# Performance work log

Measured on AMD Instinct MI355X. Metric: run time of the kernel, lower is better.

The kernel has to match this reference:

```python
import jax, jax.numpy as jnp
import numpy as np

BETA_MIN, BETA_MAX = 0.01, 0.995
EPS_DELTA, EPS_RMS = 1e-6, 1e-5


def _rmsnorm(x, w):
    ms = jnp.mean(x * x, axis=-1, keepdims=True)
    return x * jax.lax.rsqrt(ms + EPS_RMS) * w


def _delta_scan(q, k, v, beta, mask, bb1, bb2):
    # q, k, v: [B, S, D]; beta, mask: [B, S, 1]; bb1, bb2: scalars
    phi_q = jax.nn.elu(q) + 1.0
    phi_k = jax.nn.elu(k) + 1.0
    b1_base = jnp.clip(jax.nn.sigmoid(bb1), BETA_MIN, BETA_MAX)
    b2_base = jnp.clip(jax.nn.sigmoid(bb2), BETA_MIN, BETA_MAX)
    B, S, D = q.shape

    def step(carry, inp):
        H1, H2, Z1, Z2 = carry
        qt, kt, vt, bt, mt = inp  # qt/kt/vt: [B,D], bt/mt: [B,1]
        bin_t = jnp.clip(bt, BETA_MIN, BETA_MAX)
        b1 = jnp.clip(b1_base * bin_t, BETA_MIN, BETA_MAX)  # [B,1]
        b2 = jnp.clip(b2_base * bin_t, BETA_MIN, BETA_MAX)
        kv = jnp.einsum('bd,be->bde', kt, vt) * mt[:, :, None]  # [B,D,D]
        H1 = H1 * b1[:, :, None] + kv
        H2 = H2 * b2[:, :, None] + kv
        km = kt * mt
        Z1 = Z1 * b1 + km
        Z2 = Z2 * b2 + km
        num = jnp.einsum('bd,bde->be', qt, H1 + H2)
        den = jnp.maximum(jnp.sum(qt * (Z1 + Z2), axis=-1, keepdims=True), EPS_DELTA)
        return (H1, H2, Z1, Z2), num / den * mt

    init = (jnp.zeros((B, D, D), q.dtype), jnp.zeros((B, D, D), q.dtype),
            jnp.zeros((B, D), q.dtype), jnp.zeros((B, D), q.dtype))
    xs = tuple(a.swapaxes(0, 1) for a in (phi_q, phi_k, v, beta, mask))
    _, outs = jax.lax.scan(step, init, xs)
    return outs.swapaxes(0, 1)  # [B, S, D]


def setup_inputs() -> dict:
    key = jax.random.key(0)
    B, S, Dm, H = 4, 2048, 512, 8
    ks = jax.random.split(key, 8)
    scale = float(1.0 / np.sqrt(Dm))
    return {
        'x': jax.random.normal(ks[0], (B, S, Dm), jnp.float32),
        'mask': jnp.ones((B, S), jnp.float32),
        'Wq': jax.random.normal(ks[1], (Dm, Dm), jnp.float32) * scale,
        'Wk': jax.random.normal(ks[2], (Dm, Dm), jnp.float32) * scale,
        'Wv': jax.random.normal(ks[3], (Dm, Dm), jnp.float32) * scale,
        'Wb': jax.random.normal(ks[4], (H, Dm), jnp.float32) * scale,
        'bb': jnp.full((H,), 1.5, jnp.float32),
        'Wo': jax.random.normal(ks[5], (Dm, Dm), jnp.float32) * scale,
        'bo': jnp.zeros((Dm,), jnp.float32),
        'ln_w': jnp.ones((Dm,), jnp.float32),
        'recency': jnp.zeros((H,), jnp.float32),
        'base_beta_1': jnp.asarray(2.0, jnp.float32),
        'base_beta_2': jnp.asarray(3.0, jnp.float32),
    }


def reference(x, mask, Wq, Wk, Wv, Wb, bb, Wo, bo, ln_w, recency,
              base_beta_1, base_beta_2):
    B, S, Dm = x.shape
    H = recency.shape[0]
    d = Dm // H
    h = _rmsnorm(x, ln_w)
    q = h @ Wq.T
    k = h @ Wk.T
    v = h @ Wv.T
    # input-conditioned gate with per-head recency bias  -> [B, S, H]
    beta = jax.nn.sigmoid(h @ Wb.T + bb + recency)

    def to_heads(t):  # [B,S,Dm] -> [B*H, S, d]
        return t.reshape(B, S, H, d).transpose(0, 2, 1, 3).reshape(B * H, S, d)

    qh, kh, vh = to_heads(q), to_heads(k), to_heads(v)
    betah = beta.transpose(0, 2, 1).reshape(B * H, S, 1)
    maskh = jnp.broadcast_to(mask[:, None, :, None], (B, H, S, 1)).reshape(B * H, S, 1)
    o = _delta_scan(qh, kh, vh, betah, maskh, base_beta_1, base_beta_2)
    o = o.reshape(B, H, S, d).transpose(0, 2, 1, 3).reshape(B, S, Dm)
    return x + (o @ Wo.T + bo)
```

## Files before the change

kernel.cpp:

```cpp
#include <hip/hip_runtime.h>
#include <stdint.h>

typedef unsigned short u16;
typedef short bf16x8 __attribute__((ext_vector_type(8)));
typedef unsigned short u16x8 __attribute__((ext_vector_type(8)));
typedef unsigned short u16x4 __attribute__((ext_vector_type(4)));
typedef float f32x4 __attribute__((ext_vector_type(4)));

#define S_ 2048
#define DM 512
#define DH 64
#define CL 64
#define NCH 32

#define SW(r, sc) ((r) * 72 + ((sc) ^ (((r) & 7) << 3)))

__device__ __forceinline__ float b2f(u16 u) { return __uint_as_float(((unsigned)u) << 16); }
__device__ __forceinline__ u16 f2b(float f) {
    unsigned v = __float_as_uint(f);
    unsigned r = v + 0x7fffu + ((v >> 16) & 1u);
    return (u16)(r >> 16);
}
__device__ __forceinline__ float phi_elu(float x) { return x > 0.f ? x + 1.f : __expf(x); }
__device__ __forceinline__ float clip01(float v) { return fminf(fmaxf(v, 0.01f), 0.995f); }

__device__ __forceinline__ void gload16(const u16* g, u16* l) {
    __builtin_amdgcn_global_load_lds((const __attribute__((address_space(1))) void*)g,
                                     (__attribute__((address_space(3))) void*)l, 16, 0, 0);
}

__global__ __launch_bounds__(256) void k_rbw(const float* __restrict__ x, const float* __restrict__ lnw,
                                             const float* __restrict__ Wb, const float* __restrict__ bb,
                                             const float* __restrict__ rec, const float* __restrict__ bb1p,
                                             const float* __restrict__ bb2p, u16* __restrict__ h,
                                             float* __restrict__ lb1, float* __restrict__ lb2,
                                             const float* __restrict__ Wq, const float* __restrict__ Wk,
                                             const float* __restrict__ Wv, const float* __restrict__ Wo,
                                             u16* __restrict__ wcat, u16* __restrict__ wo) {
    if (blockIdx.x >= 2048) {
        int idx = (blockIdx.x - 2048) * 256 + threadIdx.x;
        int e0 = idx << 2;
        if (e0 < 1536 * 512) {
            int r = e0 >> 9, ccol = e0 & 511;
            const float* src = (r < 512) ? (Wq + (size_t)r * 512)
                             : (r < 1024) ? (Wk + (size_t)(r - 512) * 512)
                                          : (Wv + (size_t)(r - 1024) * 512);
            float4 v = *(const float4*)(src + ccol);
            u16x4 o = {f2b(v.x), f2b(v.y), f2b(v.z), f2b(v.w)};
            *(u16x4*)(wcat + e0) = o;
        } else {
            int e = e0 - 1536 * 512;
            float4 v = *(const float4*)(Wo + e);
            u16x4 o = {f2b(v.x), f2b(v.y), f2b(v.z), f2b(v.w)};
            *(u16x4*)(wo + e) = o;
        }
        return;
    }
    int wave = threadIdx.x >> 6, lane = threadIdx.x & 63;
    int row = blockIdx.x * 4 + wave;
    const float* xr = x + (size_t)row * DM + lane * 8;
    float4 v0 = *(const float4*)xr;
    float4 v1 = *(const float4*)(xr + 4);
    float ss = v0.x * v0.x + v0.y * v0.y + v0.z * v0.z + v0.w * v0.w +
               v1.x * v1.x + v1.y * v1.y + v1.z * v1.z + v1.w * v1.w;
    #pragma unroll
    for (int off = 32; off; off >>= 1) ss += __shfl_xor(ss, off, 64);
    float sc = rsqrtf(ss * (1.f / DM) + 1e-5f);
    const float* wr_ = lnw + lane * 8;
    float4 w0 = *(const float4*)wr_;
    float4 w1 = *(const float4*)(wr_ + 4);
    float hv[8];
    hv[0] = v0.x * sc * w0.x; hv[1] = v0.y * sc * w0.y;
    hv[2] = v0.z * sc * w0.z; hv[3] = v0.w * sc * w0.w;
    hv[4] = v1.x * sc * w1.x; hv[5] = v1.y * sc * w1.y;
    hv[6] = v1.z * sc * w1.z; hv[7] = v1.w * sc * w1.w;
    u16x8 o;
    #pragma unroll
    for (int j = 0; j < 8; j++) o[j] = f2b(hv[j]);
    *(u16x8*)(h + (size_t)row * DM + lane * 8) = o;
    float acc[8];
    #pragma unroll
    for (int hd = 0; hd < 8; hd++) {
        const float* wp = Wb + hd * DM + lane * 8;
        float4 a0 = *(const float4*)wp;
        float4 a1 = *(const float4*)(wp + 4);
        acc[hd] = hv[0] * a0.x + hv[1] * a0.y + hv[2] * a0.z + hv[3] * a0.w +
                  hv[4] * a1.x + hv[5] * a1.y + hv[6] * a1.z + hv[7] * a1.w;
    }
    #pragma unroll
    for (int hd = 0; hd < 8; hd++) {
        #pragma unroll
        for (int off = 32; off; off >>= 1) acc[hd] += __shfl_xor(acc[hd], off, 64);
    }
    if (lane == 0) {
        float b1b = clip01(1.f / (1.f + __expf(-bb1p[0])));
        float b2b = clip01(1.f / (1.f + __expf(-bb2p[0])));
        int b = row >> 11, s = row & 2047;
        #pragma unroll
        for (int hd = 0; hd < 8; hd++) {
            float logit = acc[hd] + bb[hd] + rec[hd];
            float beta = 1.f / (1.f + __expf(-logit));
            float bin = clip01(beta);
            float b1 = clip01(b1b * bin);
            float b2 = clip01(b2b * bin);
            size_t o2 = (size_t)((b << 3) + hd) * S_ + s;
            lb1[o2] = log2f(b1);
            lb2[o2] = log2f(b2);
        }
    }
}

template<int MODE, int NT, int BM>
__global__ __launch_bounds__(BM * 2) void k_gemm(const u16* __restrict__ A, const u16* __restrict__ Bw, int K,
                                                 const float* __restrict__ mask, u16* __restrict__ qh,
                                                 u16* __restrict__ kh, u16* __restrict__ vh,
                                                 const float* __restrict__ xres, const float* __restrict__ bo,
                                                 float* __restrict__ outp) {
    constexpr int THREADS = BM * 2;
    constexpr int RPC = THREADS / 8;
    constexpr int ACALLS = BM / RPC;
    constexpr int BCALLS = 128 / RPC;
    __shared__ u16 SH[BM * 64 + 128 * 64];
    u16* As = SH;
    u16* Bs = SH + BM * 64;
    int tid = threadIdx.x;
    int lane = tid & 63, w = tid >> 6;
    int wr = w >> 1, wc = w & 1;
    int hwid = blockIdx.y * gridDim.x + blockIdx.x;
    int nwg = gridDim.x * NT;
    int q8 = nwg >> 3;
    int logical = (hwid & 7) * q8 + (hwid >> 3);
    int mTile = logical / NT, nTile = logical % NT;
    int m0 = mTile * BM, n0 = nTile * 128;
    f32x4 acc[4][4] = {};
    int r0 = tid >> 3;
    int swc8 = ((lane & 7) ^ (lane >> 3)) << 3;
    const u16* gA0 = A + (size_t)(m0 + r0) * K + swc8;
    const u16* gB0 = Bw + (size_t)(n0 + r0) * K + swc8;
    u16* lA = As + w * 512;
    u16* lB = Bs + w * 512;
    int l15 = lane & 15;
    int kgrp = lane >> 4;
    for (int k0 = 0; k0 < K; k0 += 64) {
        if (k0) __syncthreads();
        #pragma unroll
        for (int rb = 0; rb < ACALLS; rb++)
            gload16(gA0 + (size_t)rb * RPC * K + k0, lA + rb * RPC * 64);
        #pragma unroll
        for (int rb = 0; rb < BCALLS; rb++)
            gload16(gB0 + (size_t)rb * RPC * K + k0, lB + rb * RPC * 64);
        __syncthreads();
        #pragma unroll
        for (int kk = 0; kk < 2; kk++) {
            int kg = kgrp + kk * 4;
            int cg = (kg ^ (l15 & 7)) << 3;
            bf16x8 af[4], bfr[4];
            #pragma unroll
            for (int m = 0; m < 4; m++) af[m] = *(const bf16x8*)&As[(wr * 64 + m * 16 + l15) * 64 + cg];
            #pragma unroll
            for (int n = 0; n < 4; n++) bfr[n] = *(const bf16x8*)&Bs[(wc * 64 + n * 16 + l15) * 64 + cg];
            #pragma unroll
            for (int m = 0; m < 4; m++)
                #pragma unroll
                for (int n = 0; n < 4; n++)
                    acc[m][n] = __builtin_amdgcn_mfma_f32_16x16x32_bf16(af[m], bfr[n], acc[m][n], 0, 0, 0);
        }
    }
    __syncthreads();
    if constexpr (MODE == 0) {
        int mat = n0 >> 9;
        int cb = n0 & 511;
        u16* basep = (mat == 0) ? qh : (mat == 1) ? kh : vh;
        #pragma unroll
        for (int P = 0; P < BM / 64; P++) {
            if (wr == P) {
                #pragma unroll
                for (int m = 0; m < 4; m++)
                    #pragma unroll
                    for (int n = 0; n < 4; n++)
                        #pragma unroll
                        for (int r = 0; r < 4; r++) {
                            int rl = m * 16 + ((lane >> 4) << 2) + r;
                            int colL = wc * 64 + n * 16 + l15;
                            SH[rl * 140 + colL] = f2b(acc[m][n][r]);
                        }
            }
            __syncthreads();
            {
                int rl = tid >> 2;
                int gr = m0 + P * 64 + rl;
                int b = gr >> 11, s = gr & 2047;
                float mv = (mat == 1) ? mask[(b << 11) + s] : 1.f;
                #pragma unroll
                for (int cc = 0; cc < 4; cc++) {
                    int cl = ((tid & 3) << 5) + (cc << 3);
                    u16x8 vv = *(const u16x8*)&SH[rl * 140 + cl];
                    int f = cb + cl;
                    int hh = f >> 6, j = f & 63;
                    u16* dst = basep + ((size_t)(b * 8 + hh) * S_ + s) * DH + j;
                    if (mat == 2) {
                        *(u16x8*)dst = vv;
                    } else {
                        u16x8 ov;
                        #pragma unroll
                        for (int e = 0; e < 8; e++) {
                            float v = b2f(vv[e]);
                            ov[e] = f2b(phi_elu(v) * mv);
                        }
                        *(u16x8*)dst = ov;
                    }
                }
            }
            __syncthreads();
        }
    } else {
        float* SF = (float*)SH;
        constexpr int PQN = BM / 32;
        #pragma unroll
        for (int Pq = 0; Pq < PQN; Pq++) {
            if (wr == (Pq >> 1)) {
                int mbase = (Pq & 1) * 2;
                #pragma unroll
                for (int mm = 0; mm < 2; mm++)
                    #pragma unroll
                    for (int n = 0; n < 4; n++)
                        #pragma unroll
                        for (int r = 0; r < 4; r++) {
                            int rl = mm * 16 + ((lane >> 4) << 2) + r;
                            int colL = wc * 64 + n * 16 + l15;
                            SF[rl * 136 + colL] = acc[mbase + mm][n][r];
                        }
            }
            __syncthreads();
            {
                int rl, col0;
                if constexpr (THREADS == 256) { rl = tid >> 3; col0 = (tid & 7) << 4; }
                else                          { rl = tid >> 2; col0 = (tid & 3) << 5; }
                constexpr int NCC = (THREADS == 256) ? 4 : 8;
                int gr = m0 + Pq * 32 + rl;
                const float* xr = xres + (size_t)gr * DM + n0 + col0;
                float* orow = outp + (size_t)gr * DM + n0 + col0;
                #pragma unroll
                for (int cc = 0; cc < NCC; cc++) {
                    int cl = col0 + (cc << 2);
                    float4 v = *(const float4*)&SF[rl * 136 + cl];
                    float4 xv = *(const float4*)(xr + (cc << 2));
                    float4 bv = *(const float4*)(bo + n0 + cl);
                    float4 ov = {v.x + xv.x + bv.x, v.y + xv.y + bv.y,
                                 v.z + xv.z + bv.z, v.w + xv.w + bv.w};
                    *(float4*)(orow + (cc << 2)) = ov;
                }
            }
            __syncthreads();
        }
    }
}

__global__ __launch_bounds__(256) void k_pass1(const u16* __restrict__ kh, const u16* __restrict__ vh,
                                               const float* __restrict__ lb1, const float* __restrict__ lb2,
                                               u16* __restrict__ S1b, u16* __restrict__ S2b,
                                               float* __restrict__ z1, float* __restrict__ z2,
                                               float* __restrict__ P1, float* __restrict__ P2) {
    __shared__ u16 Kw1[64 * 72];
    __shared__ u16 Kw2[64 * 72];
    __shared__ u16 Vt[64 * 72];
    __shared__ float Ls1[64], Ls2[64];
    int tid = threadIdx.x;
    int bh = blockIdx.x >> 5, c = blockIdx.x & 31;
    int wave = tid >> 6, lane = tid & 63;
    size_t base = ((size_t)bh * S_ + c * CL) * DH;
    if (wave == 0) {
        float v = lb1[(size_t)bh * S_ + c * CL + lane];
        #pragma unroll
        for (int d = 1; d < 64; d <<= 1) { float o = __shfl_up(v, d, 64); if (lane >= d) v += o; }
        Ls1[lane] = v;
    } else if (wave == 1) {
        float v = lb2[(size_t)bh * S_ + c * CL + lane];
        #pragma unroll
        for (int d = 1; d < 64; d <<= 1) { float o = __shfl_up(v, d, 64); if (lane >= d) v += o; }
        Ls2[lane] = v;
    }
    int ss = tid & 63, i0 = (tid >> 6) << 4;
    const u16* kr = kh + base + (size_t)ss * DH + i0;
    u16x8 kk0 = *(const u16x8*)kr;
    u16x8 kk1 = *(const u16x8*)(kr + 8);
    {
        const u16* vr = vh + base + (size_t)ss * DH + i0;
        u16x8 vv0 = *(const u16x8*)vr;
        u16x8 vv1 = *(const u16x8*)(vr + 8);
        #pragma unroll
        for (int j = 0; j < 8; j++) {
            Vt[SW(i0 + j, ss)] = vv0[j];
            Vt[SW(i0 + 8 + j, ss)] = vv1[j];
        }
    }
    __syncthreads();
    float w1 = exp2f(Ls1[63] - Ls1[ss]);
    float w2 = exp2f(Ls2[63] - Ls2[ss]);
    #pragma unroll
    for (int j = 0; j < 8; j++) {
        float k0 = b2f(kk0[j]), k1 = b2f(kk1[j]);
        Kw1[SW(i0 + j, ss)] = f2b(w1 * k0);
        Kw2[SW(i0 + j, ss)] = f2b(w2 * k0);
        Kw1[SW(i0 + 8 + j, ss)] = f2b(w1 * k1);
        Kw2[SW(i0 + 8 + j, ss)] = f2b(w2 * k1);
    }
    if (tid == 0) { P1[blockIdx.x] = exp2f(Ls1[63]); P2[blockIdx.x] = exp2f(Ls2[63]); }
    __syncthreads();
    int l15 = lane & 15, kh8 = (lane >> 4) << 3;
    int j0 = wave << 4;
    bf16x8 vf0 = *(const bf16x8*)&Vt[SW(j0 + l15, kh8)];
    bf16x8 vf1 = *(const bf16x8*)&Vt[SW(j0 + l15, 32 + kh8)];
    f32x4 a1[4], a2[4];
    #pragma unroll
    for (int it = 0; it < 4; it++) { a1[it] = (f32x4){0,0,0,0}; a2[it] = (f32x4){0,0,0,0}; }
    #pragma unroll
    for (int it = 0; it < 4; it++) {
        int ir = (it << 4) + l15;
        bf16x8 b0 = *(const bf16x8*)&Kw1[SW(ir, kh8)];
        bf16x8 b1 = *(const bf16x8*)&Kw1[SW(ir, 32 + kh8)];
        a1[it] = __builtin_amdgcn_mfma_f32_16x16x32_bf16(vf0, b0, a1[it], 0, 0, 0);
        a1[it] = __builtin_amdgcn_mfma_f32_16x16x32_bf16(vf1, b1, a1[it], 0, 0, 0);
        bf16x8 c0 = *(const bf16x8*)&Kw2[SW(ir, kh8)];
        bf16x8 c1 = *(const bf16x8*)&Kw2[SW(ir, 32 + kh8)];
        a2[it] = __builtin_amdgcn_mfma_f32_16x16x32_bf16(vf0, c0, a2[it], 0, 0, 0);
        a2[it] = __builtin_amdgcn_mfma_f32_16x16x32_bf16(vf1, c1, a2[it], 0, 0, 0);
    }
    {
        int iz = tid >> 2, sg = tid & 3;
        u16x8 x0 = *(const u16x8*)&Kw1[SW(iz, sg << 4)];
        u16x8 x1 = *(const u16x8*)&Kw1[SW(iz, (sg << 4) + 8)];
        u16x8 y0 = *(const u16x8*)&Kw2[SW(iz, sg << 4)];
        u16x8 y1 = *(const u16x8*)&Kw2[SW(iz, (sg << 4) + 8)];
        float z1v = 0.f, z2v = 0.f;
        #pragma unroll
        for (int j = 0; j < 8; j++) {
            z1v += b2f(x0[j]) + b2f(x1[j]);
            z2v += b2f(y0[j]) + b2f(y1[j]);
        }
        z1v += __shfl_xor(z1v, 1, 64); z1v += __shfl_xor(z1v, 2, 64);
        z2v += __shfl_xor(z2v, 1, 64); z2v += __shfl_xor(z2v, 2, 64);
        if (sg == 0) {
            z1[(size_t)blockIdx.x * 64 + iz] = z1v;
            z2[(size_t)blockIdx.x * 64 + iz] = z2v;
        }
    }
    int jr0 = j0 + ((lane >> 4) << 2);
    size_t so = (size_t)blockIdx.x * 4096;
    #pragma unroll
    for (int it = 0; it < 4; it++) {
        int ii = (it << 4) + l15;
        #pragma unroll
        for (int r = 0; r < 4; r++) {
            S1b[so + (size_t)(jr0 + r) * 64 + ii] = f2b(a1[it][r]);
            S2b[so + (size_t)(jr0 + r) * 64 + ii] = f2b(a2[it][r]);
        }
    }
}

__global__ __launch_bounds__(256) void k_pass2(u16* __restrict__ S1b, u16* __restrict__ S2b,
                                               float* __restrict__ z1, float* __restrict__ z2,
                                               const float* __restrict__ P1, const float* __restrict__ P2) {
    int blk = blockIdx.x;
    if (blk < 512) {
        int bh = blk >> 4;
        int e = ((blk & 15) << 8) + threadIdx.x;
        float c1 = 0.f, c2 = 0.f;
        #pragma unroll 4
        for (int c = 0; c < NCH; c++) {
            int bc = bh * NCH + c;
            size_t idx = (size_t)bc * 4096 + e;
            float p1 = P1[bc], p2 = P2[bc];
            float t1 = b2f(S1b[idx]); S1b[idx] = f2b(c1); c1 = c1 * p1 + t1;
            float t2 = b2f(S2b[idx]); S2b[idx] = f2b(c2); c2 = c2 * p2 + t2;
        }
    } else {
        int bh = ((blk - 512) << 2) + (threadIdx.x >> 6);
        int e = threadIdx.x & 63;
        float y1 = 0.f, y2 = 0.f;
        #pragma unroll 4
        for (int c = 0; c < NCH; c++) {
            int bc = bh * NCH + c;
            size_t zi = (size_t)bc * 64 + e;
            float p1 = P1[bc], p2 = P2[bc];
            float t1 = z1[zi]; z1[zi] = y1; y1 = y1 * p1 + t1;
            float t2 = z2[zi]; z2[zi] = y2; y2 = y2 * p2 + t2;
        }
    }
}

__global__ __launch_bounds__(256) void k_pass3(const u16* __restrict__ qh, const u16* __restrict__ kh,
                                               const u16* __restrict__ vh, const float* __restrict__ lb1,
                                               const float* __restrict__ lb2, const u16* __restrict__ S1b,
                                               const u16* __restrict__ S2b, const float* __restrict__ z1,
                                               const float* __restrict__ z2, const float* __restrict__ mask,
                                               u16* __restrict__ obf) {
    __shared__ u16 Vt[64 * 72];
    __shared__ u16 AWs[64 * 72];
    __shared__ float Ls1[64], Ls2[64], dens[64], qZ1[64], qZ2[64];
    int tid = threadIdx.x;
    int bh = blockIdx.x >> 5, c = blockIdx.x & 31;
    int wave = tid >> 6, lane = tid & 63;
    size_t base = ((size_t)bh * S_ + c * CL) * DH;
    if (wave == 0) {
        float v = lb1[(size_t)bh * S_ + c * CL + lane];
        #pragma unroll
        for (int d = 1; d < 64; d <<= 1) { float o = __shfl_up(v, d, 64); if (lane >= d) v += o; }
        Ls1[lane] = v;
    } else if (wave == 1) {
        float v = lb2[(size_t)bh * S_ + c * CL + lane];
        #pragma unroll
        for (int d = 1; d < 64; d <<= 1) { float o = __shfl_up(v, d, 64); if (lane >= d) v += o; }
        Ls2[lane] = v;
    }
    {
        int ss = tid & 63, i0 = (tid >> 6) << 4;
        const u16* vr = vh + base + (size_t)ss * DH + i0;
        u16x8 vv0 = *(const u16x8*)vr;
        u16x8 vv1 = *(const u16x8*)(vr + 8);
        #pragma unroll
        for (int j = 0; j < 8; j++) {
            Vt[SW(i0 + j, ss)] = vv0[j];
            Vt[SW(i0 + 8 + j, ss)] = vv1[j];
        }
    }
    {
        int t = tid >> 2, g = tid & 3;
        const u16* qp = qh + base + (size_t)t * DH + (g << 4);
        u16x8 q0 = *(const u16x8*)qp;
        u16x8 q1 = *(const u16x8*)(qp + 8);
        const float* z1p = z1 + (size_t)blockIdx.x * 64 + (g << 4);
        const float* z2p = z2 + (size_t)blockIdx.x * 64 + (g << 4);
        float az1 = 0.f, az2 = 0.f;
        #pragma unroll
        for (int m = 0; m < 8; m++) {
            float qv0 = b2f(q0[m]), qv1 = b2f(q1[m]);
            az1 += qv0 * z1p[m] + qv1 * z1p[m + 8];
            az2 += qv0 * z2p[m] + qv1 * z2p[m + 8];
        }
        az1 += __shfl_xor(az1, 1, 64); az1 += __shfl_xor(az1, 2, 64);
        az2 += __shfl_xor(az2, 1, 64); az2 += __shfl_xor(az2, 2, 64);
        if (g == 0) { qZ1[t] = az1; qZ2[t] = az2; }
    }
    int l15 = lane & 15, kh8 = (lane >> 4) << 3;
    int t0 = wave << 4;
    const u16* qb = qh + base + (size_t)(t0 + l15) * DH;
    bf16x8 qf0 = *(const bf16x8*)(qb + kh8);
    bf16x8 qf1 = *(const bf16x8*)(qb + 32 + kh8);
    f32x4 accA[4];
    #pragma unroll
    for (int st = 0; st < 4; st++) accA[st] = (f32x4){0, 0, 0, 0};
    #pragma unroll
    for (int st = 0; st < 4; st++) {
        const u16* kb = kh + base + (size_t)((st << 4) + l15) * DH;
        bf16x8 kf0 = *(const bf16x8*)(kb + kh8);
        bf16x8 kf1 = *(const bf16x8*)(kb + 32 + kh8);
        accA[st] = __builtin_amdgcn_mfma_f32_16x16x32_bf16(qf0, kf0, accA[st], 0, 0, 0);
        accA[st] = __builtin_amdgcn_mfma_f32_16x16x32_bf16(qf1, kf1, accA[st], 0, 0, 0);
    }
    __syncthreads();
    int trow = t0 + ((lane >> 4) << 2);
    float l1t[4], l2t[4];
    #pragma unroll
    for (int r = 0; r < 4; r++) { l1t[r] = Ls1[trow + r]; l2t[r] = Ls2[trow + r]; }
    float rs[4] = {0.f, 0.f, 0.f, 0.f};
    #pragma unroll
    for (int st = 0; st < 4; st++) {
        int s = (st << 4) + l15;
        float s1 = Ls1[s], s2 = Ls2[s];
        #pragma unroll
        for (int r = 0; r < 4; r++) {
            float w = 0.f;
            if (s <= trow + r) w = exp2f(l1t[r] - s1) + exp2f(l2t[r] - s2);
            u16 awb = f2b(accA[st][r] * w);
            AWs[SW(trow + r, s)] = awb;
            rs[r] += b2f(awb);
        }
    }
    #pragma unroll
    for (int off = 1; off < 16; off <<= 1) {
        #pragma unroll
        for (int r = 0; r < 4; r++) rs[r] += __shfl_xor(rs[r], off, 64);
    }
    if (l15 == 0) {
        #pragma unroll
        for (int r = 0; r < 4; r++) dens[trow + r] = rs[r];
    }
    __syncthreads();
    bf16x8 awf0 = *(const bf16x8*)&AWs[SW(t0 + l15, kh8)];
    bf16x8 awf1 = *(const bf16x8*)&AWs[SW(t0 + l15, 32 + kh8)];
    const u16* h1g = S1b + (size_t)blockIdx.x * 4096;
    const u16* h2g = S2b + (size_t)blockIdx.x * 4096;
    f32x4 accO[4], accC1[4], accC2[4];
    #pragma unroll
    for (int jt = 0; jt < 4; jt++) {
        accO[jt] = (f32x4){0, 0, 0, 0};
        accC1[jt] = (f32x4){0, 0, 0, 0};
        accC2[jt] = (f32x4){0, 0, 0, 0};
    }
    #pragma unroll
    for (int jt = 0; jt < 4; jt++) {
        int jr = (jt << 4) + l15;
        bf16x8 v0 = *(const bf16x8*)&Vt[SW(jr, kh8)];
        bf16x8 v1 = *(const bf16x8*)&Vt[SW(jr, 32 + kh8)];
        accO[jt] = __builtin_amdgcn_mfma_f32_16x16x32_bf16(awf0, v0, accO[jt], 0, 0, 0);
        accO[jt] = __builtin_amdgcn_mfma_f32_16x16x32_bf16(awf1, v1, accO[jt], 0, 0, 0);
        bf16x8 h10 = *(const bf16x8*)(h1g + (size_t)jr * 64 + kh8);
        bf16x8 h11 = *(const bf16x8*)(h1g + (size_t)jr * 64 + 32 + kh8);
        accC1[jt] = __builtin_amdgcn_mfma_f32_16x16x32_bf16(qf0, h10, accC1[jt], 0, 0, 0);
        accC1[jt] = __builtin_amdgcn_mfma_f32_16x16x32_bf16(qf1, h11, accC1[jt], 0, 0, 0);
        bf16x8 h20 = *(const bf16x8*)(h2g + (size_t)jr * 64 + kh8);
        bf16x8 h21 = *(const bf16x8*)(h2g + (size_t)jr * 64 + 32 + kh8);
        accC2[jt] = __builtin_amdgcn_mfma_f32_16x16x32_bf16(qf0, h20, accC2[jt], 0, 0, 0);
        accC2[jt] = __builtin_amdgcn_mfma_f32_16x16x32_bf16(qf1, h21, accC2[jt], 0, 0, 0);
    }
    int b = bh >> 3, hh = bh & 7;
    #pragma unroll
    for (int r = 0; r < 4; r++) {
        int t = trow + r;
        float e1 = exp2f(l1t[r]), e2 = exp2f(l2t[r]);
        float den = dens[t] + e1 * qZ1[t] + e2 * qZ2[t];
        den = fmaxf(den, 1e-6f);
        int sg = (c << 6) + t;
        float mv = mask[(size_t)b * S_ + sg];
        float inv = mv / den;
        u16* op = obf + ((size_t)b * S_ + sg) * DM + hh * DH;
        #pragma unroll
        for (int jt = 0; jt < 4; jt++) {
            float numv = accO[jt][r] + e1 * accC1[jt][r] + e2 * accC2[jt][r];
            op[(jt << 4) + l15] = f2b(numv * inv);
        }
    }
}

extern "C" void kernel_launch(void* const* d_in, const int* in_sizes, int n_in,
                              void* d_out, int out_size, void* d_ws, size_t ws_size,
                              hipStream_t stream) {
    const float* x    = (const float*)d_in[0];
    const float* mask = (const float*)d_in[1];
    const float* Wq   = (const float*)d_in[2];
    const float* Wk   = (const float*)d_in[3];
    const float* Wv   = (const float*)d_in[4];
    const float* Wb   = (const float*)d_in[5];
    const float* bb   = (const float*)d_in[6];
    const float* Wo   = (const float*)d_in[7];
    const float* bo   = (const float*)d_in[8];
    const float* lnw  = (const float*)d_in[9];
    const float* rec  = (const float*)d_in[10];
    const float* bb1  = (const float*)d_in[11];
    const float* bb2  = (const float*)d_in[12];
    float* out = (float*)d_out;

    char* w = (char*)d_ws;
    u16* h    = (u16*)w;  w += (size_t)8192 * 512 * 2;
    u16* wcat = (u16*)w;  w += (size_t)1536 * 512 * 2;
    u16* wo   = (u16*)w;  w += (size_t)512 * 512 * 2;
    u16* qh   = (u16*)w;  w += (size_t)8192 * 512 * 2;
    u16* kh   = (u16*)w;  w += (size_t)8192 * 512 * 2;
    u16* vh   = (u16*)w;  w += (size_t)8192 * 512 * 2;
    float* lb1 = (float*)w; w += (size_t)32 * 2048 * 4;
    float* lb2 = (float*)w; w += (size_t)32 * 2048 * 4;
    u16* S1b  = (u16*)w;  w += (size_t)1024 * 4096 * 2;
    u16* S2b  = (u16*)w;  w += (size_t)1024 * 4096 * 2;
    float* z1  = (float*)w; w += (size_t)1024 * 64 * 4;
    float* z2  = (float*)w; w += (size_t)1024 * 64 * 4;
    float* P1  = (float*)w; w += 4096;
    float* P2  = (float*)w; w += 4096;
    u16* obf   = (u16*)w;   w += (size_t)8192 * 512 * 2;

    k_rbw<<<3072, 256, 0, stream>>>(x, lnw, Wb, bb, rec, bb1, bb2, h, lb1, lb2,
                                    Wq, Wk, Wv, Wo, wcat, wo);
    k_gemm<0, 12, 128><<<dim3(64, 12), 256, 0, stream>>>(h, wcat, 512, mask, qh, kh, vh, nullptr, nullptr, nullptr);
    k_pass1<<<1024, 256, 0, stream>>>(kh, vh, lb1, lb2, S1b, S2b, z1, z2, P1, P2);
    k_pass2<<<520, 256, 0, stream>>>(S1b, S2b, z1, z2, P1, P2);
    k_pass3<<<1024, 256, 0, stream>>>(qh, kh, vh, lb1, lb2, S1b, S2b, z1, z2, mask, obf);
    k_gemm<1, 4, 64><<<dim3(128, 4), 128, 0, stream>>>(obf, wo, 512, nullptr, nullptr, nullptr, nullptr, x, bo, out);
}
```

Baseline: 100.1 us.

## Fuse three-pass chunked scan into single sequential per-head kernel

The three chunked-scan kernels (chunk state computation, cross-chunk prefix, output) are replaced by one kernel with one block per batch-head. That block walks all 32 chunks in order and carries the running states H1/H2 and Z in registers and shared memory. This removes the global round-trips of the per-chunk states and two launches. The cost is that only 32 blocks run, so most of the GPU sits idle during the serial chunk loop. The output GEMM is also switched to the 128-row, 256-thread configuration.

```diff
diff --git a/kernel.cpp b/kernel.cpp
--- a/kernel.cpp
+++ b/kernel.cpp
@@ -233,15 +233,13 @@
             }
             __syncthreads();
             {
-                int rl, col0;
-                if constexpr (THREADS == 256) { rl = tid >> 3; col0 = (tid & 7) << 4; }
-                else                          { rl = tid >> 2; col0 = (tid & 3) << 5; }
-                constexpr int NCC = (THREADS == 256) ? 4 : 8;
+                int rl = tid >> 3;
+                int col0 = (tid & 7) << 4;
                 int gr = m0 + Pq * 32 + rl;
                 const float* xr = xres + (size_t)gr * DM + n0 + col0;
                 float* orow = outp + (size_t)gr * DM + n0 + col0;
                 #pragma unroll
-                for (int cc = 0; cc < NCC; cc++) {
+                for (int cc = 0; cc < 4; cc++) {
                     int cl = col0 + (cc << 2);
                     float4 v = *(const float4*)&SF[rl * 136 + cl];
                     float4 xv = *(const float4*)(xr + (cc << 2));
@@ -256,280 +254,229 @@
     }
 }
 
-__global__ __launch_bounds__(256) void k_pass1(const u16* __restrict__ kh, const u16* __restrict__ vh,
-                                               const float* __restrict__ lb1, const float* __restrict__ lb2,
-                                               u16* __restrict__ S1b, u16* __restrict__ S2b,
-                                               float* __restrict__ z1, float* __restrict__ z2,
-                                               float* __restrict__ P1, float* __restrict__ P2) {
+__global__ __launch_bounds__(512) void k_scan(const u16* __restrict__ qh, const u16* __restrict__ kh,
+                                              const u16* __restrict__ vh, const float* __restrict__ lb1,
+                                              const float* __restrict__ lb2, const float* __restrict__ mask,
+                                              u16* __restrict__ obf) {
+    __shared__ u16 Vt[64 * 72];
     __shared__ u16 Kw1[64 * 72];
     __shared__ u16 Kw2[64 * 72];
-    __shared__ u16 Vt[64 * 72];
-    __shared__ float Ls1[64], Ls2[64];
+    __shared__ u16 AWs[64 * 72];
+    __shared__ u16 H1s[64 * 72];
+    __shared__ u16 H2s[64 * 72];
+    __shared__ float Ls1[64], Ls2[64], dens[64], qZ1[64], qZ2[64], zE1[64], zE2[64];
     int tid = threadIdx.x;
-    int bh = blockIdx.x >> 5, c = blockIdx.x & 31;
+    int bh = blockIdx.x;
     int wave = tid >> 6, lane = tid & 63;
-    size_t base = ((size_t)bh * S_ + c * CL) * DH;
-    if (wave == 0) {
-        float v = lb1[(size_t)bh * S_ + c * CL + lane];
-        #pragma unroll
-        for (int d = 1; d < 64; d <<= 1) { float o = __shfl_up(v, d, 64); if (lane >= d) v += o; }
-        Ls1[lane] = v;
-    } else if (wave == 1) {
-        float v = lb2[(size_t)bh * S_ + c * CL + lane];
-        #pragma unroll
-        for (int d = 1; d < 64; d <<= 1) { float o = __shfl_up(v, d, 64); if (lane >= d) v += o; }
-        Ls2[lane] = v;
-    }
-    int ss = tid & 63, i0 = (tid >> 6) << 4;
-    const u16* kr = kh + base + (size_t)ss * DH + i0;
-    u16x8 kk0 = *(const u16x8*)kr;
-    u16x8 kk1 = *(const u16x8*)(kr + 8);
-    {
-        const u16* vr = vh + base + (size_t)ss * DH + i0;
-        u16x8 vv0 = *(const u16x8*)vr;
-        u16x8 vv1 = *(const u16x8*)(vr + 8);
-        #pragma unroll
-        for (int j = 0; j < 8; j++) {
-            Vt[SW(i0 + j, ss)] = vv0[j];
-            Vt[SW(i0 + 8 + j, ss)] = vv1[j];
-        }
-    }
+    int l15 = lane & 15, kh8 = (lane >> 4) << 3;
+    int b = bh >> 3, hh = bh & 7;
+    for (int i = tid; i < 64 * 72; i += 512) { H1s[i] = 0; H2s[i] = 0; }
+    if (tid < 64) { zE1[tid] = 0.f; zE2[tid] = 0.f; }
+    f32x4 h1r[4], h2r[4];
+    #pragma unroll
+    for (int it = 0; it < 4; it++) { h1r[it] = (f32x4){0,0,0,0}; h2r[it] = (f32x4){0,0,0,0}; }
     __syncthreads();
-    float w1 = exp2f(Ls1[63] - Ls1[ss]);
-    float w2 = exp2f(Ls2[63] - Ls2[ss]);
-    #pragma unroll
-    for (int j = 0; j < 8; j++) {
-        float k0 = b2f(kk0[j]), k1 = b2f(kk1[j]);
-        Kw1[SW(i0 + j, ss)] = f2b(w1 * k0);
-        Kw2[SW(i0 + j, ss)] = f2b(w2 * k0);
-        Kw1[SW(i0 + 8 + j, ss)] = f2b(w1 * k1);
-        Kw2[SW(i0 + 8 + j, ss)] = f2b(w2 * k1);
-    }
-    if (tid == 0) { P1[blockIdx.x] = exp2f(Ls1[63]); P2[blockIdx.x] = exp2f(Ls2[63]); }
-    __syncthreads();
-    int l15 = lane & 15, kh8 = (lane >> 4) << 3;
-    int j0 = wave << 4;
-    bf16x8 vf0 = *(const bf16x8*)&Vt[SW(j0 + l15, kh8)];
-    bf16x8 vf1 = *(const bf16x8*)&Vt[SW(j0 + l15, 32 + kh8)];
-    f32x4 a1[4], a2[4];
-    #pragma unroll
-    for (int it = 0; it < 4; it++) { a1[it] = (f32x4){0,0,0,0}; a2[it] = (f32x4){0,0,0,0}; }
-    #pragma unroll
-    for (int it = 0; it < 4; it++) {
-        int ir = (it << 4) + l15;
-        bf16x8 b0 = *(const bf16x8*)&Kw1[SW(ir, kh8)];
-        bf16x8 b1 = *(const bf16x8*)&Kw1[SW(ir, 32 + kh8)];
-        a1[it] = __builtin_amdgcn_mfma_f32_16x16x32_bf16(vf0, b0, a1[it], 0, 0, 0);
-        a1[it] = __builtin_amdgcn_mfma_f32_16x16x32_bf16(vf1, b1, a1[it], 0, 0, 0);
-        bf16x8 c0 = *(const bf16x8*)&Kw2[SW(ir, kh8)];
-        bf16x8 c1 = *(const bf16x8*)&Kw2[SW(ir, 32 + kh8)];
-        a2[it] = __builtin_amdgcn_mfma_f32_16x16x32_bf16(vf0, c0, a2[it], 0, 0, 0);
-        a2[it] = __builtin_amdgcn_mfma_f32_16x16x32_bf16(vf1, c1, a2[it], 0, 0, 0);
-    }
-    {
-        int iz = tid >> 2, sg = tid & 3;
-        u16x8 x0 = *(const u16x8*)&Kw1[SW(iz, sg << 4)];
-        u16x8 x1 = *(const u16x8*)&Kw1[SW(iz, (sg << 4) + 8)];
-        u16x8 y0 = *(const u16x8*)&Kw2[SW(iz, sg << 4)];
-        u16x8 y1 = *(const u16x8*)&Kw2[SW(iz, (sg << 4) + 8)];
+
+    for (int c = 0; c < NCH; c++) {
+        size_t base = ((size_t)bh * S_ + (size_t)c * CL) * DH;
+        int ss = tid & 63, i0 = (tid >> 6) << 3;
+        u16x8 kk = *(const u16x8*)(kh + base + (size_t)ss * DH + i0);
+        {
+            u16x8 vv = *(const u16x8*)(vh + base + (size_t)ss * DH + i0);
+            #pragma unroll
+            for (int j = 0; j < 8; j++) Vt[SW(i0 + j, ss)] = vv[j];
+        }
+        if (wave == 0) {
+            float v = lb1[(size_t)bh * S_ + c * CL + lane];
+            #pragma unroll
+            for (int d = 1; d < 64; d <<= 1) { float o = __shfl_up(v, d, 64); if (lane >= d) v += o; }
+            Ls1[lane] = v;
+        } else if (wave == 1) {
+            float v = lb2[(size_t)bh * S_ + c * CL + lane];
+            #pragma unroll
+            for (int d = 1; d < 64; d <<= 1) { float o = __shfl_up(v, d, 64); if (lane >= d) v += o; }
+            Ls2[lane] = v;
+        }
+        __syncthreads();
+        {
+            float w1 = exp2f(Ls1[63] - Ls1[ss]);
+            float w2 = exp2f(Ls2[63] - Ls2[ss]);
+            #pragma unroll
+            for (int j = 0; j < 8; j++) {
+                float kf = b2f(kk[j]);
+                Kw1[SW(i0 + j, ss)] = f2b(w1 * kf);
+                Kw2[SW(i0 + j, ss)] = f2b(w2 * kf);
+            }
+        }
+        f32x4 accA[4];
+        bf16x8 qf0, qf1;
+        if (wave < 4) {
+            int t0 = wave << 4;
+            const u16* qb = qh + base + (size_t)(t0 + l15) * DH;
+            qf0 = *(const bf16x8*)(qb + kh8);
+            qf1 = *(const bf16x8*)(qb + 32 + kh8);
+            #pragma unroll
+            for (int st = 0; st < 4; st++) accA[st] = (f32x4){0, 0, 0, 0};
+            #pragma unroll
+            for (int st = 0; st < 4; st++) {
+                const u16* kb = kh + base + (size_t)((st << 4) + l15) * DH;
+                bf16x8 kf0 = *(const bf16x8*)(kb + kh8);
+                bf16x8 kf1 = *(const bf16x8*)(kb + 32 + kh8);
+                accA[st] = __builtin_amdgcn_mfma_f32_16x16x32_bf16(qf0, kf0, accA[st], 0, 0, 0);
+                accA[st] = __builtin_amdgcn_mfma_f32_16x16x32_bf16(qf1, kf1, accA[st], 0, 0, 0);
+            }
+        } else {
+            int local = tid - 256;
+            int t = local >> 2, g = local & 3;
+            const u16* qp = qh + base + (size_t)t * DH + (g << 4);
+            u16x8 q0 = *(const u16x8*)qp;
+            u16x8 q1 = *(const u16x8*)(qp + 8);
+            float az1 = 0.f, az2 = 0.f;
+            #pragma unroll
+            for (int m = 0; m < 8; m++) {
+                float qv0 = b2f(q0[m]), qv1 = b2f(q1[m]);
+                az1 += qv0 * zE1[(g << 4) + m] + qv1 * zE1[(g << 4) + m + 8];
+                az2 += qv0 * zE2[(g << 4) + m] + qv1 * zE2[(g << 4) + m + 8];
+            }
+            az1 += __shfl_xor(az1, 1, 64); az1 += __shfl_xor(az1, 2, 64);
+            az2 += __shfl_xor(az2, 1, 64); az2 += __shfl_xor(az2, 2, 64);
+            if (g == 0) { qZ1[t] = az1; qZ2[t] = az2; }
+        }
+        __syncthreads();
+        f32x4 a1[4], a2[4];
+        float l1t[4], l2t[4];
+        int trow = 0;
+        if (wave < 4) {
+            int t0 = wave << 4;
+            trow = t0 + ((lane >> 4) << 2);
+            #pragma unroll
+            for (int r = 0; r < 4; r++) { l1t[r] = Ls1[trow + r]; l2t[r] = Ls2[trow + r]; }
+            float rs[4] = {0.f, 0.f, 0.f, 0.f};
+            #pragma unroll
+            for (int st = 0; st < 4; st++) {
+                int s = (st << 4) + l15;
+                float s1 = Ls1[s], s2 = Ls2[s];
+                #pragma unroll
+                for (int r = 0; r < 4; r++) {
+                    float w = 0.f;
+                    if (s <= trow + r) w = exp2f(l1t[r] - s1) + exp2f(l2t[r] - s2);
+                    u16 awb = f2b(accA[st][r] * w);
+                    AWs[SW(trow + r, s)] = awb;
+                    rs[r] += b2f(awb);
+                }
+            }
+            #pragma unroll
+            for (int off = 1; off < 16; off <<= 1) {
+                #pragma unroll
+                for (int r = 0; r < 4; r++) rs[r] += __shfl_xor(rs[r], off, 64);
+            }
+            if (l15 == 0) {
+                #pragma unroll
+                for (int r = 0; r < 4; r++) dens[trow + r] = rs[r];
+            }
+        } else {
+            int j0 = (wave - 4) << 4;
+            bf16x8 vf0 = *(const bf16x8*)&Vt[SW(j0 + l15, kh8)];
+            bf16x8 vf1 = *(const bf16x8*)&Vt[SW(j0 + l15, 32 + kh8)];
+            #pragma unroll
+            for (int it = 0; it < 4; it++) { a1[it] = (f32x4){0,0,0,0}; a2[it] = (f32x4){0,0,0,0}; }
+            #pragma unroll
+            for (int it = 0; it < 4; it++) {
+                int ir = (it << 4) + l15;
+                bf16x8 b0 = *(const bf16x8*)&Kw1[SW(ir, kh8)];
+                bf16x8 b1 = *(const bf16x8*)&Kw1[SW(ir, 32 + kh8)];
+                a1[it] = __builtin_amdgcn_mfma_f32_16x16x32_bf16(vf0, b0, a1[it], 0, 0, 0);
+                a1[it] = __builtin_amdgcn_mfma_f32_16x16x32_bf16(vf1, b1, a1[it], 0, 0, 0);
+                bf16x8 c0 = *(const bf16x8*)&Kw2[SW(ir, kh8)];
+                bf16x8 c1 = *(const bf16x8*)&Kw2[SW(ir, 32 + kh8)];
+                a2[it] = __builtin_amdgcn_mfma_f32_16x16x32_bf16(vf0, c0, a2[it], 0, 0, 0);
+                a2[it] = __builtin_amdgcn_mfma_f32_16x16x32_bf16(vf1, c1, a2[it], 0, 0, 0);
+            }
+        }
+        __syncthreads();
         float z1v = 0.f, z2v = 0.f;
-        #pragma unroll
-        for (int j = 0; j < 8; j++) {
-            z1v += b2f(x0[j]) + b2f(x1[j]);
-            z2v += b2f(y0[j]) + b2f(y1[j]);
-        }
-        z1v += __shfl_xor(z1v, 1, 64); z1v += __shfl_xor(z1v, 2, 64);
-        z2v += __shfl_xor(z2v, 1, 64); z2v += __shfl_xor(z2v, 2, 64);
-        if (sg == 0) {
-            z1[(size_t)blockIdx.x * 64 + iz] = z1v;
-            z2[(size_t)blockIdx.x * 64 + iz] = z2v;
-        }
-    }
-    int jr0 = j0 + ((lane >> 4) << 2);
-    size_t so = (size_t)blockIdx.x * 4096;
-    #pragma unroll
-    for (int it = 0; it < 4; it++) {
-        int ii = (it << 4) + l15;
-        #pragma unroll
-        for (int r = 0; r < 4; r++) {
-            S1b[so + (size_t)(jr0 + r) * 64 + ii] = f2b(a1[it][r]);
-            S2b[so + (size_t)(jr0 + r) * 64 + ii] = f2b(a2[it][r]);
-        }
-    }
-}
-
-__global__ __launch_bounds__(256) void k_pass2(u16* __restrict__ S1b, u16* __restrict__ S2b,
-                                               float* __restrict__ z1, float* __restrict__ z2,
-                                               const float* __restrict__ P1, const float* __restrict__ P2) {
-    int blk = blockIdx.x;
-    if (blk < 512) {
-        int bh = blk >> 4;
-        int e = ((blk & 15) << 8) + threadIdx.x;
-        float c1 = 0.f, c2 = 0.f;
-        #pragma unroll 4
-        for (int c = 0; c < NCH; c++) {
-            int bc = bh * NCH + c;
-            size_t idx = (size_t)bc * 4096 + e;
-            float p1 = P1[bc], p2 = P2[bc];
-            float t1 = b2f(S1b[idx]); S1b[idx] = f2b(c1); c1 = c1 * p1 + t1;
-            float t2 = b2f(S2b[idx]); S2b[idx] = f2b(c2); c2 = c2 * p2 + t2;
-        }
-    } else {
-        int bh = ((blk - 512) << 2) + (threadIdx.x >> 6);
-        int e = threadIdx.x & 63;
-        float y1 = 0.f, y2 = 0.f;
-        #pragma unroll 4
-        for (int c = 0; c < NCH; c++) {
-            int bc = bh * NCH + c;
-            size_t zi = (size_t)bc * 64 + e;
-            float p1 = P1[bc], p2 = P2[bc];
-            float t1 = z1[zi]; z1[zi] = y1; y1 = y1 * p1 + t1;
-            float t2 = z2[zi]; z2[zi] = y2; y2 = y2 * p2 + t2;
-        }
-    }
-}
-
-__global__ __launch_bounds__(256) void k_pass3(const u16* __restrict__ qh, const u16* __restrict__ kh,
-                                               const u16* __restrict__ vh, const float* __restrict__ lb1,
-                                               const float* __restrict__ lb2, const u16* __restrict__ S1b,
-                                               const u16* __restrict__ S2b, const float* __restrict__ z1,
-                                               const float* __restrict__ z2, const float* __restrict__ mask,
-                                               u16* __restrict__ obf) {
-    __shared__ u16 Vt[64 * 72];
-    __shared__ u16 AWs[64 * 72];
-    __shared__ float Ls1[64], Ls2[64], dens[64], qZ1[64], qZ2[64];
-    int tid = threadIdx.x;
-    int bh = blockIdx.x >> 5, c = blockIdx.x & 31;
-    int wave = tid >> 6, lane = tid & 63;
-    size_t base = ((size_t)bh * S_ + c * CL) * DH;
-    if (wave == 0) {
-        float v = lb1[(size_t)bh * S_ + c * CL + lane];
-        #pragma unroll
-        for (int d = 1; d < 64; d <<= 1) { float o = __shfl_up(v, d, 64); if (lane >= d) v += o; }
-        Ls1[lane] = v;
-    } else if (wave == 1) {
-        float v = lb2[(size_t)bh * S_ + c * CL + lane];
-        #pragma unroll
-        for (int d = 1; d < 64; d <<= 1) { float o = __shfl_up(v, d, 64); if (lane >= d) v += o; }
-        Ls2[lane] = v;
-    }
-    {
-        int ss = tid & 63, i0 = (tid >> 6) << 4;
-        const u16* vr = vh + base + (size_t)ss * DH + i0;
-        u16x8 vv0 = *(const u16x8*)vr;
-        u16x8 vv1 = *(const u16x8*)(vr + 8);
-        #pragma unroll
-        for (int j = 0; j < 8; j++) {
-            Vt[SW(i0 + j, ss)] = vv0[j];
-            Vt[SW(i0 + 8 + j, ss)] = vv1[j];
-        }
-    }
-    {
-        int t = tid >> 2, g = tid & 3;
-        const u16* qp = qh + base + (size_t)t * DH + (g << 4);
-        u16x8 q0 = *(const u16x8*)qp;
-        u16x8 q1 = *(const u16x8*)(qp + 8);
-        const float* z1p = z1 + (size_t)blockIdx.x * 64 + (g << 4);
-        const float* z2p = z2 + (size_t)blockIdx.x * 64 + (g << 4);
-        float az1 = 0.f, az2 = 0.f;
-        #pragma unroll
-        for (int m = 0; m < 8; m++) {
-            float qv0 = b2f(q0[m]), qv1 = b2f(q1[m]);
-            az1 += qv0 * z1p[m] + qv1 * z1p[m + 8];
-            az2 += qv0 * z2p[m] + qv1 * z2p[m + 8];
-        }
-        az1 += __shfl_xor(az1, 1, 64); az1 += __shfl_xor(az1, 2, 64);
-        az2 += __shfl_xor(az2, 1, 64); az2 += __shfl_xor(az2, 2, 64);
-        if (g == 0) { qZ1[t] = az1; qZ2[t] = az2; }
-    }
-    int l15 = lane & 15, kh8 = (lane >> 4) << 3;
-    int t0 = wave << 4;
-    const u16* qb = qh + base + (size_t)(t0 + l15) * DH;
-    bf16x8 qf0 = *(const bf16x8*)(qb + kh8);
-    bf16x8 qf1 = *(const bf16x8*)(qb + 32 + kh8);
-    f32x4 accA[4];
-    #pragma unroll
-    for (int st = 0; st < 4; st++) accA[st] = (f32x4){0, 0, 0, 0};
-    #pragma unroll
-    for (int st = 0; st < 4; st++) {
-        const u16* kb = kh + base + (size_t)((st << 4) + l15) * DH;
-        bf16x8 kf0 = *(const bf16x8*)(kb + kh8);
-        bf16x8 kf1 = *(const bf16x8*)(kb + 32 + kh8);
-        accA[st] = __builtin_amdgcn_mfma_f32_16x16x32_bf16(qf0, kf0, accA[st], 0, 0, 0);
-        accA[st] = __builtin_amdgcn_mfma_f32_16x16x32_bf16(qf1, kf1, accA[st], 0, 0, 0);
-    }
-    __syncthreads();
-    int trow = t0 + ((lane >> 4) << 2);
-    float l1t[4], l2t[4];
-    #pragma unroll
-    for (int r = 0; r < 4; r++) { l1t[r] = Ls1[trow + r]; l2t[r] = Ls2[trow + r]; }
-    float rs[4] = {0.f, 0.f, 0.f, 0.f};
-    #pragma unroll
-    for (int st = 0; st < 4; st++) {
-        int s = (st << 4) + l15;
-        float s1 = Ls1[s], s2 = Ls2[s];
-        #pragma unroll
-        for (int r = 0; r < 4; r++) {
-            float w = 0.f;
-            if (s <= trow + r) w = exp2f(l1t[r] - s1) + exp2f(l2t[r] - s2);
-            u16 awb = f2b(accA[st][r] * w);
-            AWs[SW(trow + r, s)] = awb;
-            rs[r] += b2f(awb);
-        }
-    }
-    #pragma unroll
-    for (int off = 1; off < 16; off <<= 1) {
-        #pragma unroll
-        for (int r = 0; r < 4; r++) rs[r] += __shfl_xor(rs[r], off, 64);
-    }
-    if (l15 == 0) {
-        #pragma unroll
-        for (int r = 0; r < 4; r++) dens[trow + r] = rs[r];
-    }
-    __syncthreads();
-    bf16x8 awf0 = *(const bf16x8*)&AWs[SW(t0 + l15, kh8)];
-    bf16x8 awf1 = *(const bf16x8*)&AWs[SW(t0 + l15, 32 + kh8)];
-    const u16* h1g = S1b + (size_t)blockIdx.x * 4096;
-    const u16* h2g = S2b + (size_t)blockIdx.x * 4096;
-    f32x4 accO[4], accC1[4], accC2[4];
-    #pragma unroll
-    for (int jt = 0; jt < 4; jt++) {
-        accO[jt] = (f32x4){0, 0, 0, 0};
-        accC1[jt] = (f32x4){0, 0, 0, 0};
-        accC2[jt] = (f32x4){0, 0, 0, 0};
-    }
-    #pragma unroll
-    for (int jt = 0; jt < 4; jt++) {
-        int jr = (jt << 4) + l15;
-        bf16x8 v0 = *(const bf16x8*)&Vt[SW(jr, kh8)];
-        bf16x8 v1 = *(const bf16x8*)&Vt[SW(jr, 32 + kh8)];
-        accO[jt] = __builtin_amdgcn_mfma_f32_16x16x32_bf16(awf0, v0, accO[jt], 0, 0, 0);
-        accO[jt] = __builtin_amdgcn_mfma_f32_16x16x32_bf16(awf1, v1, accO[jt], 0, 0, 0);
-        bf16x8 h10 = *(const bf16x8*)(h1g + (size_t)jr * 64 + kh8);
-        bf16x8 h11 = *(const bf16x8*)(h1g + (size_t)jr * 64 + 32 + kh8);
-        accC1[jt] = __builtin_amdgcn_mfma_f32_16x16x32_bf16(qf0, h10, accC1[jt], 0, 0, 0);
-        accC1[jt] = __builtin_amdgcn_mfma_f32_16x16x32_bf16(qf1, h11, accC1[jt], 0, 0, 0);
-        bf16x8 h20 = *(const bf16x8*)(h2g + (size_t)jr * 64 + kh8);
-        bf16x8 h21 = *(const bf16x8*)(h2g + (size_t)jr * 64 + 32 + kh8);
-        accC2[jt] = __builtin_amdgcn_mfma_f32_16x16x32_bf16(qf0, h20, accC2[jt], 0, 0, 0);
-        accC2[jt] = __builtin_amdgcn_mfma_f32_16x16x32_bf16(qf1, h21, accC2[jt], 0, 0, 0);
-    }
-    int b = bh >> 3, hh = bh & 7;
-    #pragma unroll
-    for (int r = 0; r < 4; r++) {
-        int t = trow + r;
-        float e1 = exp2f(l1t[r]), e2 = exp2f(l2t[r]);
-        float den = dens[t] + e1 * qZ1[t] + e2 * qZ2[t];
-        den = fmaxf(den, 1e-6f);
-        int sg = (c << 6) + t;
-        float mv = mask[(size_t)b * S_ + sg];
-        float inv = mv / den;
-        u16* op = obf + ((size_t)b * S_ + sg) * DM + hh * DH;
-        #pragma unroll
-        for (int jt = 0; jt < 4; jt++) {
-            float numv = accO[jt][r] + e1 * accC1[jt][r] + e2 * accC2[jt][r];
-            op[(jt << 4) + l15] = f2b(numv * inv);
-        }
+        if (wave < 4) {
+            int t0 = wave << 4;
+            bf16x8 awf0 = *(const bf16x8*)&AWs[SW(t0 + l15, kh8)];
+            bf16x8 awf1 = *(const bf16x8*)&AWs[SW(t0 + l15, 32 + kh8)];
+            f32x4 accO[4], accC1[4], accC2[4];
+            #pragma unroll
+            for (int jt = 0; jt < 4; jt++) {
+                accO[jt] = (f32x4){0, 0, 0, 0};
+                accC1[jt] = (f32x4){0, 0, 0, 0};
+                accC2[jt] = (f32x4){0, 0, 0, 0};
+            }
+            #pragma unroll
+            for (int jt = 0; jt < 4; jt++) {
+                int jr = (jt << 4) + l15;
+                bf16x8 v0 = *(const bf16x8*)&Vt[SW(jr, kh8)];
+                bf16x8 v1 = *(const bf16x8*)&Vt[SW(jr, 32 + kh8)];
+                accO[jt] = __builtin_amdgcn_mfma_f32_16x16x32_bf16(awf0, v0, accO[jt], 0, 0, 0);
+                accO[jt] = __builtin_amdgcn_mfma_f32_16x16x32_bf16(awf1, v1, accO[jt], 0, 0, 0);
+                bf16x8 h10 = *(const bf16x8*)&H1s[SW(jr, kh8)];
+                bf16x8 h11 = *(const bf16x8*)&H1s[SW(jr, 32 + kh8)];
+                accC1[jt] = __builtin_amdgcn_mfma_f32_16x16x32_bf16(qf0, h10, accC1[jt], 0, 0, 0);
+                accC1[jt] = __builtin_amdgcn_mfma_f32_16x16x32_bf16(qf1, h11, accC1[jt], 0, 0, 0);
+                bf16x8 h20 = *(const bf16x8*)&H2s[SW(jr, kh8)];
+                bf16x8 h21 = *(const bf16x8*)&H2s[SW(jr, 32 + kh8)];
+                accC2[jt] = __builtin_amdgcn_mfma_f32_16x16x32_bf16(qf0, h20, accC2[jt], 0, 0, 0);
+                accC2[jt] = __builtin_amdgcn_mfma_f32_16x16x32_bf16(qf1, h21, accC2[jt], 0, 0, 0);
+            }
+            #pragma unroll
+            for (int r = 0; r < 4; r++) {
+                int t = trow + r;
+                float e1 = exp2f(l1t[r]), e2 = exp2f(l2t[r]);
+                float den = dens[t] + e1 * qZ1[t] + e2 * qZ2[t];
+                den = fmaxf(den, 1e-6f);
+                int sg = (c << 6) + t;
+                float mv = mask[(size_t)b * S_ + sg];
+                float inv = mv / den;
+                u16* op = obf + ((size_t)b * S_ + sg) * DM + hh * DH;
+                #pragma unroll
+                for (int jt = 0; jt < 4; jt++) {
+                    float numv = accO[jt][r] + e1 * accC1[jt][r] + e2 * accC2[jt][r];
+                    op[(jt << 4) + l15] = f2b(numv * inv);
+                }
+            }
+        } else {
+            int local = tid - 256;
+            int iz = local >> 2, sg = local & 3;
+            u16x8 x0 = *(const u16x8*)&Kw1[SW(iz, sg << 4)];
+            u16x8 x1 = *(const u16x8*)&Kw1[SW(iz, (sg << 4) + 8)];
+            u16x8 y0 = *(const u16x8*)&Kw2[SW(iz, sg << 4)];
+            u16x8 y1 = *(const u16x8*)&Kw2[SW(iz, (sg << 4) + 8)];
+            #pragma unroll
+            for (int j = 0; j < 8; j++) {
+                z1v += b2f(x0[j]) + b2f(x1[j]);
+                z2v += b2f(y0[j]) + b2f(y1[j]);
+            }
+            z1v += __shfl_xor(z1v, 1, 64); z1v += __shfl_xor(z1v, 2, 64);
+            z2v += __shfl_xor(z2v, 1, 64); z2v += __shfl_xor(z2v, 2, 64);
+        }
+        __syncthreads();
+        if (wave >= 4) {
+            float p1 = exp2f(Ls1[63]), p2 = exp2f(Ls2[63]);
+            int j0 = (wave - 4) << 4;
+            int jr0 = j0 + ((lane >> 4) << 2);
+            #pragma unroll
+            for (int it = 0; it < 4; it++) {
+                int ii = (it << 4) + l15;
+                #pragma unroll
+                for (int r = 0; r < 4; r++) {
+                    h1r[it][r] = h1r[it][r] * p1 + a1[it][r];
+                    h2r[it][r] = h2r[it][r] * p2 + a2[it][r];
+                    H1s[SW(jr0 + r, ii)] = f2b(h1r[it][r]);
+                    H2s[SW(jr0 + r, ii)] = f2b(h2r[it][r]);
+                }
+            }
+            int local = tid - 256;
+            int iz = local >> 2, sg = local & 3;
+            if (sg == 0) {
+                zE1[iz] = zE1[iz] * p1 + z1v;
+                zE2[iz] = zE2[iz] * p2 + z2v;
+            }
+        }
+        __syncthreads();
     }
 }
 
@@ -560,19 +507,11 @@
     u16* vh   = (u16*)w;  w += (size_t)8192 * 512 * 2;
     float* lb1 = (float*)w; w += (size_t)32 * 2048 * 4;
     float* lb2 = (float*)w; w += (size_t)32 * 2048 * 4;
-    u16* S1b  = (u16*)w;  w += (size_t)1024 * 4096 * 2;
-    u16* S2b  = (u16*)w;  w += (size_t)1024 * 4096 * 2;
-    float* z1  = (float*)w; w += (size_t)1024 * 64 * 4;
-    float* z2  = (float*)w; w += (size_t)1024 * 64 * 4;
-    float* P1  = (float*)w; w += 4096;
-    float* P2  = (float*)w; w += 4096;
     u16* obf   = (u16*)w;   w += (size_t)8192 * 512 * 2;
 
     k_rbw<<<3072, 256, 0, stream>>>(x, lnw, Wb, bb, rec, bb1, bb2, h, lb1, lb2,
                                     Wq, Wk, Wv, Wo, wcat, wo);
     k_gemm<0, 12, 128><<<dim3(64, 12), 256, 0, stream>>>(h, wcat, 512, mask, qh, kh, vh, nullptr, nullptr, nullptr);
-    k_pass1<<<1024, 256, 0, stream>>>(kh, vh, lb1, lb2, S1b, S2b, z1, z2, P1, P2);
-    k_pass2<<<520, 256, 0, stream>>>(S1b, S2b, z1, z2, P1, P2);
-    k_pass3<<<1024, 256, 0, stream>>>(qh, kh, vh, lb1, lb2, S1b, S2b, z1, z2, mask, obf);
-    k_gemm<1, 4, 64><<<dim3(128, 4), 128, 0, stream>>>(obf, wo, 512, nullptr, nullptr, nullptr, nullptr, x, bo, out);
+    k_scan<<<32, 512, 0, stream>>>(qh, kh, vh, lb1, lb2, mask, obf);
+    k_gemm<1, 4, 128><<<dim3(64, 4), 256, 0, stream>>>(obf, wo, 512, nullptr, nullptr, nullptr, nullptr, x, bo, out);
 }
```

New measurement: 319.9 us. +219.5%, slower.
